# Kernel optimization log

Hardware: AMD Instinct MI355X
Metric: run time of the kernel (lower is better)

Reference implementation:

```python
import jax, jax.numpy as jnp
import numpy as np

N_NODES = 50000
N_EDGES = 1_600_000
D_IN = 128
D_HID = 128
N_CLASSES = 8
N_GRAPHS = 64


def setup_inputs() -> dict:
    key = jax.random.key(0)
    ks = jax.random.split(key, 8)
    x = jax.random.normal(ks[0], (N_NODES, D_IN), dtype=jnp.float32)
    edge_index = jax.random.randint(ks[1], (2, N_EDGES), 0, N_NODES, dtype=jnp.int32)
    graph_ids = jnp.sort(jax.random.randint(ks[2], (N_NODES,), 0, N_GRAPHS, dtype=jnp.int32))
    s = 1.0 / np.sqrt(D_HID)
    W1 = jax.random.normal(ks[3], (D_IN, D_HID), dtype=jnp.float32) * s
    b1 = jnp.zeros((D_HID,), dtype=jnp.float32)
    W2 = jax.random.normal(ks[4], (D_HID, D_HID), dtype=jnp.float32) * s
    b2 = jnp.zeros((D_HID,), dtype=jnp.float32)
    Wc = jax.random.normal(ks[5], (D_HID, N_CLASSES), dtype=jnp.float32) * s
    bc = jnp.zeros((N_CLASSES,), dtype=jnp.float32)
    return {"x": x, "edge_index": edge_index, "graph_ids": graph_ids,
            "W1": W1, "b1": b1, "W2": W2, "b2": b2, "Wc": Wc, "bc": bc}


def _gcn_layer(h, src, dst, norm, W, b):
    # message: gather source features, apply symmetric degree normalization
    msg = h[src] * norm[:, None]                       # [E, d]
    agg = jax.ops.segment_sum(msg, dst, num_segments=N_NODES)  # [N, d]
    return jax.nn.relu(agg @ W + b)


def reference(x, edge_index, graph_ids, W1, b1, W2, b2, Wc, bc):
    src, dst = edge_index[0], edge_index[1]
    ones_e = jnp.ones((N_EDGES,), dtype=x.dtype)
    deg = jax.ops.segment_sum(ones_e, dst, num_segments=N_NODES)
    deg_inv_sqrt = jnp.where(deg > 0, jax.lax.rsqrt(jnp.maximum(deg, 1.0)), 0.0)
    norm = deg_inv_sqrt[src] * deg_inv_sqrt[dst]       # [E]

    h = _gcn_layer(x, src, dst, norm, W1, b1)
    h = _gcn_layer(h, src, dst, norm, W2, b2)

    # per-graph mean pooling (segment mean over nodes of each graph)
    ones_n = jnp.ones((N_NODES,), dtype=h.dtype)
    counts = jax.ops.segment_sum(ones_n, graph_ids, num_segments=N_GRAPHS)
    pooled = jax.ops.segment_sum(h, graph_ids, num_segments=N_GRAPHS)
    pooled = pooled / jnp.maximum(counts, 1.0)[:, None]  # [G, d]

    logits = pooled @ Wc + bc                           # [G, n_classes]
    return logits
```

## Files before the change

### kernel.cpp

```cpp
#include <hip/hip_runtime.h>
#include <hip/hip_bf16.h>

#define D_HID 128
#define N_GRAPHS 64
#define N_CLASSES 8
#define NPB 16
#define CAP 96
#define KSWEEP 4


__device__ inline unsigned short f2b(float x) {
    unsigned int u = __float_as_uint(x);
    unsigned int r = (u + 0x7fffu + ((u >> 16) & 1u)) >> 16;
    return (unsigned short)r;
}
__device__ inline float b2f(unsigned short u) {
    return __uint_as_float((unsigned int)u << 16);
}

__global__ __launch_bounds__(256) void prep_kernel(const float* __restrict__ x,
                                                   uint2* __restrict__ xb4,
                                                   int castBlocks, int n4,
                                                   const int* __restrict__ src,
                                                   const int* __restrict__ dst,
                                                   int* __restrict__ cursor,
                                                   unsigned short* __restrict__ csr16,
                                                   int E, int N, int fillBlocks, int rangeSize) {
    const int b = blockIdx.x;
    if (b < castBlocks) {
        int i = b * 256 + threadIdx.x;
        if (i < n4) {
            float4 v = ((const float4*)x)[i];
            uint2 o;
            o.x = (unsigned int)f2b(v.x) | ((unsigned int)f2b(v.y) << 16);
            o.y = (unsigned int)f2b(v.z) | ((unsigned int)f2b(v.w) << 16);
            xb4[i] = o;
        }
        return;
    }
    const int fb = b - castBlocks;
    const int sweep = fb / fillBlocks;
    const int blk = fb - sweep * fillBlocks;
    const int e = blk * 256 + threadIdx.x;
    if (e >= E) return;
    const int s = src[e];
    const int lo = sweep * rangeSize;
    if (s < lo || s >= lo + rangeSize) return;
    const int d = dst[e];
    int slot = atomicAdd(&cursor[d], 1);
    if (slot < CAP) csr16[(size_t)slot * N + d] = (unsigned short)s;
}

__global__ __launch_bounds__(256) void dis_counts_kernel(const int* __restrict__ deg,
                                                         float* __restrict__ dis,
                                                         const int* __restrict__ gid,
                                                         int* __restrict__ counts, int N) {
    int n = blockIdx.x * blockDim.x + threadIdx.x;
    if (n < N) {
        int v = deg[n];
        dis[n] = (v > 0) ? rsqrtf((float)v) : 0.0f;
    }
    if (blockIdx.x == 0 && threadIdx.x < N_GRAPHS) {
        int g = threadIdx.x;
        int lo0 = 0, hi0 = N;
        while (lo0 < hi0) { int mid = (lo0 + hi0) >> 1; if (gid[mid] < g) lo0 = mid + 1; else hi0 = mid; }
        int lo1 = lo0, hi1 = N;
        while (lo1 < hi1) { int mid = (lo1 + hi1) >> 1; if (gid[mid] < g + 1) lo1 = mid + 1; else hi1 = mid; }
        counts[g] = lo1 - lo0;
    }
}

__global__ __launch_bounds__(256) void layer_kernel(const unsigned short* __restrict__ h_in,
                                                    const int* __restrict__ deg,
                                                    const unsigned short* __restrict__ csr16,
                                                    const float* __restrict__ dis,
                                                    const float* __restrict__ W,
                                                    const float* __restrict__ bias,
                                                    unsigned short* __restrict__ h_out,
                                                    float* __restrict__ pooled,
                                                    const int* __restrict__ gid,
                                                    int fuse_pool, int N) {
    const int base = blockIdx.x * NPB;
    const int tid = threadIdx.x;
    const int wv = tid >> 6;
    const int lane = tid & 63;
    const int q = lane >> 4;
    const int ql = lane & 15;
    __shared__ float s_agg[NPB][D_HID];

    const int n0 = base + wv * 4;
    float acc[4][8] = {};
    int dd[4];
    #pragma unroll
    for (int i = 0; i < 4; ++i) {
        const int n = n0 + i;
        dd[i] = (n < N) ? min(deg[n], CAP) : 0;
    }
    const int dm = max(max(dd[0], dd[1]), max(dd[2], dd[3]));

    for (int cb = 0; cb < dm; cb += 64) {
        const int cm = min(64, dm - cb);
        unsigned int pk[4];
        #pragma unroll
        for (int i = 0; i < 4; ++i) {
            pk[i] = 0u;
            if (lane < dd[i] - cb) {
                unsigned int u = (unsigned int)csr16[(size_t)(cb + lane) * N + (n0 + i)];
                pk[i] = u | ((unsigned int)f2b(dis[u]) << 16);
            }
        }
        #pragma unroll 4
        for (int j = 0; j < cm; j += 4) {
            const int e = j + q;
            #pragma unroll
            for (int i = 0; i < 4; ++i) {
                const unsigned int p = (unsigned int)__shfl((int)pk[i], e);
                const float w = __uint_as_float(p & 0xffff0000u);
                const uint4 r = *(const uint4*)&h_in[(size_t)(p & 0xffffu) * D_HID + ql * 8];
                acc[i][0] = fmaf(w, __uint_as_float(r.x << 16), acc[i][0]);
                acc[i][1] = fmaf(w, __uint_as_float(r.x & 0xffff0000u), acc[i][1]);
                acc[i][2] = fmaf(w, __uint_as_float(r.y << 16), acc[i][2]);
                acc[i][3] = fmaf(w, __uint_as_float(r.y & 0xffff0000u), acc[i][3]);
                acc[i][4] = fmaf(w, __uint_as_float(r.z << 16), acc[i][4]);
                acc[i][5] = fmaf(w, __uint_as_float(r.z & 0xffff0000u), acc[i][5]);
                acc[i][6] = fmaf(w, __uint_as_float(r.w << 16), acc[i][6]);
                acc[i][7] = fmaf(w, __uint_as_float(r.w & 0xffff0000u), acc[i][7]);
            }
        }
    }

    #pragma unroll
    for (int i = 0; i < 4; ++i) {
        #pragma unroll
        for (int k = 0; k < 8; ++k) {
            acc[i][k] += __shfl_down(acc[i][k], 32);
            acc[i][k] += __shfl_down(acc[i][k], 16);
        }
        if (q == 0) {
            const float dn = (n0 + i < N) ? dis[n0 + i] : 0.0f;
            #pragma unroll
            for (int k = 0; k < 8; ++k) s_agg[wv * 4 + i][ql * 8 + k] = acc[i][k] * dn;
        }
    }
    __syncthreads();

    const int t = tid & 127;
    const int nb = tid >> 7;
    float outv[8];
    const float bt = bias[t];
    #pragma unroll
    for (int i = 0; i < 8; ++i) outv[i] = bt;

    for (int k = 0; k < D_HID; k += 4) {
        const float w0 = W[(k + 0) * D_HID + t];
        const float w1 = W[(k + 1) * D_HID + t];
        const float w2 = W[(k + 2) * D_HID + t];
        const float w3 = W[(k + 3) * D_HID + t];
        #pragma unroll
        for (int i = 0; i < 8; ++i) {
            float4 a = *(const float4*)&s_agg[nb * 8 + i][k];
            outv[i] = fmaf(a.x, w0, outv[i]);
            outv[i] = fmaf(a.y, w1, outv[i]);
            outv[i] = fmaf(a.z, w2, outv[i]);
            outv[i] = fmaf(a.w, w3, outv[i]);
        }
    }

    #pragma unroll
    for (int i = 0; i < 8; ++i) {
        const int n = base + nb * 8 + i;
        if (n >= N) break;
        float v = fmaxf(outv[i], 0.0f);
        if (fuse_pool) {
            atomicAdd(&pooled[gid[n] * D_HID + t], v);
        } else {
            h_out[(size_t)n * D_HID + t] = f2b(v);
        }
    }
}

__global__ __launch_bounds__(128) void pool_kernel(const unsigned short* __restrict__ h,
                                                   const int* __restrict__ gid,
                                                   float* __restrict__ pooled,
                                                   int N, int nodes_per_block) {
    const int t = threadIdx.x;
    const int start = blockIdx.x * nodes_per_block;
    if (start >= N) return;
    const int endn = min(start + nodes_per_block, N);
    int cur = gid[start];
    float sum = 0.0f;
    for (int n = start; n < endn; ++n) {
        int g = gid[n];
        if (g != cur) {
            atomicAdd(&pooled[cur * D_HID + t], sum);
            cur = g; sum = 0.0f;
        }
        sum += b2f(h[(size_t)n * D_HID + t]);
    }
    atomicAdd(&pooled[cur * D_HID + t], sum);
}

__global__ __launch_bounds__(512) void classify_kernel(const float* __restrict__ pooled,
                                                       const int* __restrict__ counts,
                                                       const float* __restrict__ Wc,
                                                       const float* __restrict__ bc,
                                                       float* __restrict__ out) {
    const int g = threadIdx.x >> 3;
    const int c = threadIdx.x & 7;
    float inv = 1.0f / fmaxf((float)counts[g], 1.0f);
    float acc = bc[c];
    #pragma unroll 8
    for (int k = 0; k < D_HID; ++k) {
        acc = fmaf(pooled[g * D_HID + k] * inv, Wc[k * N_CLASSES + c], acc);
    }
    out[g * N_CLASSES + c] = acc;
}

extern "C" void kernel_launch(void* const* d_in, const int* in_sizes, int n_in,
                              void* d_out, int out_size, void* d_ws, size_t ws_size,
                              hipStream_t stream) {
    const float* x   = (const float*)d_in[0];
    const int* edge  = (const int*)d_in[1];
    const int* gid   = (const int*)d_in[2];
    const float* W1  = (const float*)d_in[3];
    const float* b1  = (const float*)d_in[4];
    const float* W2  = (const float*)d_in[5];
    const float* b2  = (const float*)d_in[6];
    const float* Wc  = (const float*)d_in[7];
    const float* bc  = (const float*)d_in[8];
    float* out       = (float*)d_out;

    const int E = in_sizes[1] / 2;
    const int N = in_sizes[2];
    const int* src = edge;
    const int* dst = edge + E;

    char* p = (char*)d_ws;
    auto take = [&](size_t bytes) {
        char* r = p;
        p += (bytes + 255) & ~(size_t)255;
        return r;
    };
    int*   cursor  = (int*)take((size_t)N * 4);
    float* dis     = (float*)take((size_t)N * 4);
    float* pooled  = (float*)take((size_t)N_GRAPHS * D_HID * 4);
    int*   counts  = (int*)take((size_t)N_GRAPHS * 4);
    unsigned short* csr16 = (unsigned short*)take((size_t)N * CAP * 2);
    unsigned short* xb  = (unsigned short*)take((size_t)N * D_HID * 2);
    unsigned short* h1b = (unsigned short*)take((size_t)N * D_HID * 2);
    size_t used = (size_t)(p - (char*)d_ws);
    size_t h2_bytes = (size_t)N * D_HID * 2;
    const bool separate_pool = (used + h2_bytes <= ws_size);
    unsigned short* h2b = separate_pool ? (unsigned short*)take(h2_bytes) : nullptr;

    hipMemsetAsync(cursor, 0, (size_t)N * 4, stream);
    hipMemsetAsync(pooled, 0, (size_t)N_GRAPHS * D_HID * 4, stream);

    const int EB = 256;
    const int n4 = (N * D_HID) / 4;
    const int castBlocks = (n4 + EB - 1) / EB;
    const int fillBlocks = (E + EB - 1) / EB;
    const int rangeSize = (N + KSWEEP - 1) / KSWEEP;
    prep_kernel<<<castBlocks + KSWEEP * fillBlocks, EB, 0, stream>>>(
        x, (uint2*)xb, castBlocks, n4, src, dst, cursor, csr16, E, N, fillBlocks, rangeSize);
    dis_counts_kernel<<<(N + EB - 1) / EB, EB, 0, stream>>>(cursor, dis, gid, counts, N);

    const int LG = (N + NPB - 1) / NPB;
    layer_kernel<<<LG, 256, 0, stream>>>(xb, cursor, csr16, dis, W1, b1, h1b, pooled, gid, 0, N);

    if (separate_pool) {
        layer_kernel<<<LG, 256, 0, stream>>>(h1b, cursor, csr16, dis, W2, b2, h2b, pooled, gid, 0, N);
        const int NPBLK = 8;
        pool_kernel<<<(N + NPBLK - 1) / NPBLK, 128, 0, stream>>>(h2b, gid, pooled, N, NPBLK);
    } else {
        layer_kernel<<<LG, 256, 0, stream>>>(h1b, cursor, csr16, dis, W2, b2, nullptr, pooled, gid, 1, N);
    }

    classify_kernel<<<1, 512, 0, stream>>>(pooled, counts, Wc, bc, out);
}
```

Baseline: 339.1 us.

## Fuse degree normalization into layers and merge pooling with classifier

```diff
diff --git a/kernel.cpp b/kernel.cpp
--- a/kernel.cpp
+++ b/kernel.cpp
@@ -7,7 +7,6 @@
 #define NPB 16
 #define CAP 96
 #define KSWEEP 4
-
 
 __device__ inline unsigned short f2b(float x) {
     unsigned int u = __float_as_uint(x);
@@ -51,35 +50,13 @@
     if (slot < CAP) csr16[(size_t)slot * N + d] = (unsigned short)s;
 }
 
-__global__ __launch_bounds__(256) void dis_counts_kernel(const int* __restrict__ deg,
-                                                         float* __restrict__ dis,
-                                                         const int* __restrict__ gid,
-                                                         int* __restrict__ counts, int N) {
-    int n = blockIdx.x * blockDim.x + threadIdx.x;
-    if (n < N) {
-        int v = deg[n];
-        dis[n] = (v > 0) ? rsqrtf((float)v) : 0.0f;
-    }
-    if (blockIdx.x == 0 && threadIdx.x < N_GRAPHS) {
-        int g = threadIdx.x;
-        int lo0 = 0, hi0 = N;
-        while (lo0 < hi0) { int mid = (lo0 + hi0) >> 1; if (gid[mid] < g) lo0 = mid + 1; else hi0 = mid; }
-        int lo1 = lo0, hi1 = N;
-        while (lo1 < hi1) { int mid = (lo1 + hi1) >> 1; if (gid[mid] < g + 1) lo1 = mid + 1; else hi1 = mid; }
-        counts[g] = lo1 - lo0;
-    }
-}
-
 __global__ __launch_bounds__(256) void layer_kernel(const unsigned short* __restrict__ h_in,
                                                     const int* __restrict__ deg,
                                                     const unsigned short* __restrict__ csr16,
-                                                    const float* __restrict__ dis,
                                                     const float* __restrict__ W,
                                                     const float* __restrict__ bias,
                                                     unsigned short* __restrict__ h_out,
-                                                    float* __restrict__ pooled,
-                                                    const int* __restrict__ gid,
-                                                    int fuse_pool, int N) {
+                                                    int N) {
     const int base = blockIdx.x * NPB;
     const int tid = threadIdx.x;
     const int wv = tid >> 6;
@@ -91,10 +68,13 @@
     const int n0 = base + wv * 4;
     float acc[4][8] = {};
     int dd[4];
+    float dnv[4];
     #pragma unroll
     for (int i = 0; i < 4; ++i) {
         const int n = n0 + i;
-        dd[i] = (n < N) ? min(deg[n], CAP) : 0;
+        const int dg = (n < N) ? deg[n] : 0;
+        dd[i] = min(dg, CAP);
+        dnv[i] = (dg > 0) ? rsqrtf((float)dg) : 0.0f;
     }
     const int dm = max(max(dd[0], dd[1]), max(dd[2], dd[3]));
 
@@ -106,7 +86,9 @@
             pk[i] = 0u;
             if (lane < dd[i] - cb) {
                 unsigned int u = (unsigned int)csr16[(size_t)(cb + lane) * N + (n0 + i)];
-                pk[i] = u | ((unsigned int)f2b(dis[u]) << 16);
+                const int du = deg[u];
+                const float wu = (du > 0) ? rsqrtf((float)du) : 0.0f;
+                pk[i] = u | ((unsigned int)f2b(wu) << 16);
             }
         }
         #pragma unroll 4
@@ -137,9 +119,8 @@
             acc[i][k] += __shfl_down(acc[i][k], 16);
         }
         if (q == 0) {
-            const float dn = (n0 + i < N) ? dis[n0 + i] : 0.0f;
             #pragma unroll
-            for (int k = 0; k < 8; ++k) s_agg[wv * 4 + i][ql * 8 + k] = acc[i][k] * dn;
+            for (int k = 0; k < 8; ++k) s_agg[wv * 4 + i][ql * 8 + k] = acc[i][k] * dnv[i];
         }
     }
     __syncthreads();
@@ -170,50 +151,47 @@
     for (int i = 0; i < 8; ++i) {
         const int n = base + nb * 8 + i;
         if (n >= N) break;
-        float v = fmaxf(outv[i], 0.0f);
-        if (fuse_pool) {
-            atomicAdd(&pooled[gid[n] * D_HID + t], v);
-        } else {
-            h_out[(size_t)n * D_HID + t] = f2b(v);
-        }
-    }
-}
-
-__global__ __launch_bounds__(128) void pool_kernel(const unsigned short* __restrict__ h,
-                                                   const int* __restrict__ gid,
-                                                   float* __restrict__ pooled,
-                                                   int N, int nodes_per_block) {
+        h_out[(size_t)n * D_HID + t] = f2b(fmaxf(outv[i], 0.0f));
+    }
+}
+
+__global__ __launch_bounds__(128) void pool_classify_kernel(const unsigned short* __restrict__ h,
+                                                            const int* __restrict__ gid,
+                                                            const float* __restrict__ Wc,
+                                                            const float* __restrict__ bc,
+                                                            float* __restrict__ out, int N) {
+    const int g = blockIdx.x;
     const int t = threadIdx.x;
-    const int start = blockIdx.x * nodes_per_block;
-    if (start >= N) return;
-    const int endn = min(start + nodes_per_block, N);
-    int cur = gid[start];
+    int lo = 0, hi = N;
+    while (lo < hi) { int mid = (lo + hi) >> 1; if (gid[mid] < g) lo = mid + 1; else hi = mid; }
+    int lo1 = lo, hi1 = N;
+    while (lo1 < hi1) { int mid = (lo1 + hi1) >> 1; if (gid[mid] < g + 1) lo1 = mid + 1; else hi1 = mid; }
+    const int cnt = lo1 - lo;
+
     float sum = 0.0f;
-    for (int n = start; n < endn; ++n) {
-        int g = gid[n];
-        if (g != cur) {
-            atomicAdd(&pooled[cur * D_HID + t], sum);
-            cur = g; sum = 0.0f;
-        }
-        sum += b2f(h[(size_t)n * D_HID + t]);
-    }
-    atomicAdd(&pooled[cur * D_HID + t], sum);
-}
-
-__global__ __launch_bounds__(512) void classify_kernel(const float* __restrict__ pooled,
-                                                       const int* __restrict__ counts,
-                                                       const float* __restrict__ Wc,
-                                                       const float* __restrict__ bc,
-                                                       float* __restrict__ out) {
-    const int g = threadIdx.x >> 3;
-    const int c = threadIdx.x & 7;
-    float inv = 1.0f / fmaxf((float)counts[g], 1.0f);
-    float acc = bc[c];
-    #pragma unroll 8
-    for (int k = 0; k < D_HID; ++k) {
-        acc = fmaf(pooled[g * D_HID + k] * inv, Wc[k * N_CLASSES + c], acc);
-    }
-    out[g * N_CLASSES + c] = acc;
+    int n = lo;
+    for (; n + 4 <= lo1; n += 4) {
+        float a0 = b2f(h[(size_t)(n + 0) * D_HID + t]);
+        float a1 = b2f(h[(size_t)(n + 1) * D_HID + t]);
+        float a2 = b2f(h[(size_t)(n + 2) * D_HID + t]);
+        float a3 = b2f(h[(size_t)(n + 3) * D_HID + t]);
+        sum += (a0 + a1) + (a2 + a3);
+    }
+    for (; n < lo1; ++n) sum += b2f(h[(size_t)n * D_HID + t]);
+
+    __shared__ float sp[D_HID];
+    sp[t] = sum;
+    __syncthreads();
+
+    if (t < N_CLASSES) {
+        const float inv = 1.0f / fmaxf((float)cnt, 1.0f);
+        float acc = bc[t];
+        #pragma unroll 8
+        for (int k = 0; k < D_HID; ++k) {
+            acc = fmaf(sp[k] * inv, Wc[k * N_CLASSES + t], acc);
+        }
+        out[g * N_CLASSES + t] = acc;
+    }
 }
 
 extern "C" void kernel_launch(void* const* d_in, const int* in_sizes, int n_in,
@@ -242,19 +220,12 @@
         return r;
     };
     int*   cursor  = (int*)take((size_t)N * 4);
-    float* dis     = (float*)take((size_t)N * 4);
-    float* pooled  = (float*)take((size_t)N_GRAPHS * D_HID * 4);
-    int*   counts  = (int*)take((size_t)N_GRAPHS * 4);
     unsigned short* csr16 = (unsigned short*)take((size_t)N * CAP * 2);
     unsigned short* xb  = (unsigned short*)take((size_t)N * D_HID * 2);
     unsigned short* h1b = (unsigned short*)take((size_t)N * D_HID * 2);
-    size_t used = (size_t)(p - (char*)d_ws);
-    size_t h2_bytes = (size_t)N * D_HID * 2;
-    const bool separate_pool = (used + h2_bytes <= ws_size);
-    unsigned short* h2b = separate_pool ? (unsigned short*)take(h2_bytes) : nullptr;
+    unsigned short* h2b = (unsigned short*)take((size_t)N * D_HID * 2);
 
     hipMemsetAsync(cursor, 0, (size_t)N * 4, stream);
-    hipMemsetAsync(pooled, 0, (size_t)N_GRAPHS * D_HID * 4, stream);
 
     const int EB = 256;
     const int n4 = (N * D_HID) / 4;
@@ -263,18 +234,10 @@
     const int rangeSize = (N + KSWEEP - 1) / KSWEEP;
     prep_kernel<<<castBlocks + KSWEEP * fillBlocks, EB, 0, stream>>>(
         x, (uint2*)xb, castBlocks, n4, src, dst, cursor, csr16, E, N, fillBlocks, rangeSize);
-    dis_counts_kernel<<<(N + EB - 1) / EB, EB, 0, stream>>>(cursor, dis, gid, counts, N);
 
     const int LG = (N + NPB - 1) / NPB;
-    layer_kernel<<<LG, 256, 0, stream>>>(xb, cursor, csr16, dis, W1, b1, h1b, pooled, gid, 0, N);
-
-    if (separate_pool) {
-        layer_kernel<<<LG, 256, 0, stream>>>(h1b, cursor, csr16, dis, W2, b2, h2b, pooled, gid, 0, N);
-        const int NPBLK = 8;
-        pool_kernel<<<(N + NPBLK - 1) / NPBLK, 128, 0, stream>>>(h2b, gid, pooled, N, NPBLK);
-    } else {
-        layer_kernel<<<LG, 256, 0, stream>>>(h1b, cursor, csr16, dis, W2, b2, nullptr, pooled, gid, 1, N);
-    }
-
-    classify_kernel<<<1, 512, 0, stream>>>(pooled, counts, Wc, bc, out);
-}
+    layer_kernel<<<LG, 256, 0, stream>>>(xb, cursor, csr16, W1, b1, h1b, N);
+    layer_kernel<<<LG, 256, 0, stream>>>(h1b, cursor, csr16, W2, b2, h2b, N);
+
+    pool_classify_kernel<<<N_GRAPHS, 128, 0, stream>>>(h2b, gid, Wc, bc, out, N);
+}
```

Result: slower. 389.3 us (+14.8%).
